# Kernel tuning notes

Hardware: AMD Instinct MI355X
Metric: run time of the kernel (lower is better)

## Reference

```python
import jax, jax.numpy as jnp
import numpy as np

K = 9        # kNN neighbors (ViG default kernel_size=9)
EPS = 1e-5   # BatchNorm eps


def _bn2d(x, gamma, beta):
    # training-mode BatchNorm2d over (B,H,W) per channel; x: [B,C,H,W]
    mean = jnp.mean(x, axis=(0, 2, 3), keepdims=True)
    var = jnp.var(x, axis=(0, 2, 3), keepdims=True)
    g = gamma.reshape(1, -1, 1, 1)
    b = beta.reshape(1, -1, 1, 1)
    return g * (x - mean) * jax.lax.rsqrt(var + EPS) + b


def setup_inputs() -> dict:
    key = jax.random.key(0)
    B, C, H, W = 8, 96, 56, 56
    oup = 192
    ks = jax.random.split(key, 8)
    sc = 0.05
    return {
        "x": jax.random.normal(ks[0], (B, C, H, W), dtype=jnp.float32),
        "W_fc1": jax.random.normal(ks[1], (C, C), dtype=jnp.float32) * sc,
        "b_fc1": jnp.zeros((C,), jnp.float32),
        "g_bn1": jnp.ones((C,), jnp.float32),
        "be_bn1": jnp.zeros((C,), jnp.float32),
        "W_edge": jax.random.normal(ks[2], (2 * C, 2 * C), dtype=jnp.float32) * sc,
        "b_edge": jnp.zeros((2 * C,), jnp.float32),
        "g_bne": jnp.ones((2 * C,), jnp.float32),
        "be_bne": jnp.zeros((2 * C,), jnp.float32),
        "W_fc2": jax.random.normal(ks[3], (2 * C, C), dtype=jnp.float32) * sc,
        "b_fc2": jnp.zeros((C,), jnp.float32),
        "g_bn2": jnp.ones((C,), jnp.float32),
        "be_bn2": jnp.zeros((C,), jnp.float32),
        "g_sabn": jnp.ones((C,), jnp.float32),
        "be_sabn": jnp.zeros((C,), jnp.float32),
        "W_dw": jax.random.normal(ks[4], (oup, C, 3, 3), dtype=jnp.float32) * sc,
        "b_dw": jnp.zeros((oup,), jnp.float32),
        "g_dwbn": jnp.ones((oup,), jnp.float32),
        "be_dwbn": jnp.zeros((oup,), jnp.float32),
    }


def reference(x, W_fc1, b_fc1, g_bn1, be_bn1, W_edge, b_edge, g_bne, be_bne,
              W_fc2, b_fc2, g_bn2, be_bn2, g_sabn, be_sabn,
              W_dw, b_dw, g_dwbn, be_dwbn):
    B, C, H, W = x.shape
    N = H * W
    shortcut = x

    # --- Grapher.fc1: 1x1 conv + BN ---
    y = jnp.einsum('bchw,cd->bdhw', x, W_fc1) + b_fc1[None, :, None, None]
    y = _bn2d(y, g_bn1, be_bn1)

    # --- dynamic kNN graph over flattened tokens ---
    ft = y.reshape(B, C, N).transpose(0, 2, 1)            # [B,N,C]
    sq = jnp.sum(ft * ft, axis=-1)                        # [B,N]
    dist = sq[:, :, None] - 2.0 * jnp.einsum('bnc,bmc->bnm', ft, ft) + sq[:, None, :]
    _, idx = jax.lax.top_k(-dist, K)                      # [B,N,K] nearest neighbors

    # --- EdgeConv: max_k act(BN(W [x_i, x_j - x_i])) ---
    x_j = jnp.take_along_axis(ft[:, :, None, :], idx[..., None], axis=1)  # [B,N,K,C]
    x_i = ft[:, :, None, :]                               # [B,N,1,C]
    e = jnp.concatenate([jnp.broadcast_to(x_i, x_j.shape), x_j - x_i], axis=-1)  # [B,N,K,2C]
    e = jnp.einsum('bnkc,cd->bnkd', e, W_edge) + b_edge
    m = jnp.mean(e, axis=(0, 1, 2))
    v = jnp.var(e, axis=(0, 1, 2))
    e = g_bne * (e - m) * jax.lax.rsqrt(v + EPS) + be_bne
    e = jax.nn.relu(e)
    g = jnp.max(e, axis=2)                                # [B,N,2C] max-aggregation

    # --- Grapher.fc2: 1x1 conv + BN, residual ---
    g = jnp.einsum('bnc,cd->bnd', g, W_fc2) + b_fc2       # [B,N,C]
    g = g.transpose(0, 2, 1).reshape(B, C, H, W)
    g = _bn2d(g, g_bn2, be_bn2)
    y = g + shortcut

    # --- SAEncoder: BN + ReLU ---
    y = jax.nn.relu(_bn2d(y, g_sabn, be_sabn))

    # --- convdw: 3x3 stride-2 conv + BN + ReLU ---
    y = jax.lax.conv_general_dilated(
        y, W_dw, window_strides=(2, 2), padding=((1, 1), (1, 1)),
        dimension_numbers=('NCHW', 'OIHW', 'NCHW')) + b_dw[None, :, None, None]
    y = jax.nn.relu(_bn2d(y, g_dwbn, be_dwbn))
    return y
```

## Files before the change

### kernel.cpp

```cpp
#include <hip/hip_runtime.h>
#include <math.h>

#define B_   8
#define C_   96
#define C2_  192
#define N_   3136
#define R_   25088
#define OUP_ 192
#define HO_  28
#define NO_  784
#define EPS_ 1e-5f
#define QS2  128
#define CAP3 64

typedef short bf16x8 __attribute__((ext_vector_type(8)));
typedef float f32x4  __attribute__((ext_vector_type(4)));

__device__ __forceinline__ int swz16(int i) { return (i & ~15) | ((i & 15) ^ ((i >> 4) & 7)); }

__global__ __launch_bounds__(512) void k_fc1_d(const float* __restrict__ x,
                                               const float* __restrict__ W1,
                                               const float* __restrict__ b1,
                                               double* __restrict__ yd) {
    __shared__ double Wl[96 * 48];
    int tid = threadIdx.x;
    int rl = tid & 255, h = tid >> 8;
    int dbase = blockIdx.y * 48;
    for (int q = tid; q < 96 * 48; q += 512) {
        int c = q / 48, dd = q % 48;
        Wl[c * 48 + dd] = (double)W1[c * 96 + dbase + dd];
    }
    __syncthreads();
    int r = blockIdx.x * 256 + rl;
    int b = r / N_;
    int n = r - b * N_;
    double acc[24];
#pragma unroll
    for (int i = 0; i < 24; i++) acc[i] = 0.0;
    const float* xp = x + (size_t)b * C_ * N_ + n;
    for (int c = 0; c < 96; ++c) {
        double xv = (double)xp[(size_t)c * N_];
        const double* w = &Wl[c * 48 + h * 24];
#pragma unroll
        for (int i = 0; i < 24; ++i) acc[i] += xv * w[i];
    }
    int d0 = dbase + h * 24;
#pragma unroll
    for (int i = 0; i < 24; i++) {
        int d = d0 + i;
        yd[((size_t)b * C_ + d) * N_ + n] = acc[i] + (double)b1[d];
    }
}

__global__ __launch_bounds__(256) void k_stats_chan_d(const double* __restrict__ src,
                                                      double* __restrict__ partial) {
    int c = blockIdx.x;
    int chunk = blockIdx.y;
    const int SPLIT = 16;
    double s = 0.0, ss = 0.0;
    for (int j = chunk * 256 + threadIdx.x; j < R_; j += SPLIT * 256) {
        int b = j / N_, n = j - b * N_;
        double v = src[((size_t)b * C_ + c) * N_ + n];
        s += v;
        ss += v * v;
    }
    __shared__ double red[8];
    for (int off = 32; off; off >>= 1) {
        s += __shfl_down(s, off, 64);
        ss += __shfl_down(ss, off, 64);
    }
    int lane = threadIdx.x & 63, w = threadIdx.x >> 6;
    if (lane == 0) { red[w * 2] = s; red[w * 2 + 1] = ss; }
    __syncthreads();
    if (threadIdx.x == 0) {
        s = red[0] + red[2] + red[4] + red[6];
        ss = red[1] + red[3] + red[5] + red[7];
        partial[(c * SPLIT + chunk) * 2] = s;
        partial[(c * SPLIT + chunk) * 2 + 1] = ss;
    }
}

__global__ void k_stats_reduce_d(const double* __restrict__ partial, double* __restrict__ stats) {
    int c = blockIdx.x * blockDim.x + threadIdx.x;
    if (c >= 96) return;
    double s = 0.0, ss = 0.0;
    for (int k = 0; k < 16; k++) {
        s += partial[(c * 16 + k) * 2];
        ss += partial[(c * 16 + k) * 2 + 1];
    }
    double m = s / (double)R_;
    double var = ss / (double)R_ - m * m;
    stats[c * 2] = m;
    stats[c * 2 + 1] = 1.0 / sqrt(var + 1e-5);
}

__global__ __launch_bounds__(256) void k_stats_chan(const float* __restrict__ src,
                                                    float* __restrict__ partial,
                                                    int Cn, int Nsp, int total) {
    int c = blockIdx.x;
    int chunk = blockIdx.y;
    int SPLIT = gridDim.y;
    float s = 0.f, ss = 0.f;
    for (int j = chunk * 256 + threadIdx.x; j < total; j += SPLIT * 256) {
        int b = j / Nsp, n = j - b * Nsp;
        float v = src[((size_t)b * Cn + c) * Nsp + n];
        s += v;
        ss += v * v;
    }
    __shared__ float red[8];
    for (int off = 32; off; off >>= 1) {
        s += __shfl_down(s, off, 64);
        ss += __shfl_down(ss, off, 64);
    }
    int lane = threadIdx.x & 63, w = threadIdx.x >> 6;
    if (lane == 0) { red[w * 2] = s; red[w * 2 + 1] = ss; }
    __syncthreads();
    if (threadIdx.x == 0) {
        s = red[0] + red[2] + red[4] + red[6];
        ss = red[1] + red[3] + red[5] + red[7];
        partial[(c * SPLIT + chunk) * 2] = s;
        partial[(c * SPLIT + chunk) * 2 + 1] = ss;
    }
}

__global__ void k_stats_reduce(const float* __restrict__ partial, float* __restrict__ stats,
                               int Cn, int SPLIT, float invcount) {
    int c = blockIdx.x * blockDim.x + threadIdx.x;
    if (c >= Cn) return;
    float s = 0.f, ss = 0.f;
    for (int k = 0; k < SPLIT; k++) {
        s += partial[(c * SPLIT + k) * 2];
        ss += partial[(c * SPLIT + k) * 2 + 1];
    }
    float m = s * invcount;
    float var = ss * invcount - m * m;
    stats[c * 2] = m;
    stats[c * 2 + 1] = 1.0f / sqrtf(var + EPS_);
}

__global__ __launch_bounds__(256) void k_stats_reduce_b2(const float* __restrict__ partial,
                                                         float* __restrict__ stats,
                                                         float invcount) {
    int c = blockIdx.x;
    float s = 0.f, ss = 0.f;
    for (int k = threadIdx.x; k < 784; k += 256) {
        s  += partial[(size_t)k * 384 + c];
        ss += partial[(size_t)k * 384 + 192 + c];
    }
    __shared__ float red[8];
    for (int off = 32; off; off >>= 1) {
        s += __shfl_down(s, off, 64);
        ss += __shfl_down(ss, off, 64);
    }
    int lane = threadIdx.x & 63, w = threadIdx.x >> 6;
    if (lane == 0) { red[w * 2] = s; red[w * 2 + 1] = ss; }
    __syncthreads();
    if (threadIdx.x == 0) {
        s = red[0] + red[2] + red[4] + red[6];
        ss = red[1] + red[3] + red[5] + red[7];
        float m = s * invcount;
        float var = ss * invcount - m * m;
        stats[c * 2] = m;
        stats[c * 2 + 1] = 1.0f / sqrtf(var + EPS_);
    }
}

__global__ __launch_bounds__(256) void k_bn1_tr(const double* __restrict__ yd,
                                                const double* __restrict__ stats,
                                                const float* __restrict__ g,
                                                const float* __restrict__ be,
                                                float* __restrict__ ftc,
                                                double* __restrict__ ftp64,
                                                unsigned short* __restrict__ fspH,
                                                double* __restrict__ sq64,
                                                float* __restrict__ sq32) {
    __shared__ double tile[64 * 97];
    __shared__ double dsq[64][4];
    int b = blockIdx.y;
    int n0 = blockIdx.x * 64;
    int tid = threadIdx.x;
    int n = tid & 63, w = tid >> 6;
    for (int k = 0; k < 24; ++k) {
        int c = k * 4 + w;
        size_t gi = ((size_t)b * C_ + c) * N_ + n0 + n;
        double m = stats[c * 2], rs = stats[c * 2 + 1];
        double v = (double)g[c] * (yd[gi] - m) * rs + (double)be[c];
        ftc[gi] = (float)v;
        tile[n * 97 + c] = v;
    }
    __syncthreads();
    int p = n, q = w;
    double vals[24];
    double s = 0.0;
    const double* lp = &tile[p * 97 + q * 24];
#pragma unroll
    for (int m2 = 0; m2 < 24; ++m2) { vals[m2] = lp[m2]; s += vals[m2] * vals[m2]; }
    dsq[p][q] = s;
    double* dst = ftp64 + ((size_t)b * N_ + n0 + p) * C_ + q * 24;
#pragma unroll
    for (int m2 = 0; m2 < 24; m2 += 2) *(double2*)&dst[m2] = make_double2(vals[m2], vals[m2 + 1]);
    unsigned* hdst = (unsigned*)(fspH + ((size_t)b * N_ + n0 + p) * QS2);
#pragma unroll
    for (int m2 = 0; m2 < 24; m2 += 2) {
        unsigned u0 = __float_as_uint((float)vals[m2]);
        unsigned u1 = __float_as_uint((float)vals[m2 + 1]);
        unsigned h0 = (u0 + 0x7fffu + ((u0 >> 16) & 1u)) >> 16;
        unsigned h1 = (u1 + 0x7fffu + ((u1 >> 16) & 1u)) >> 16;
        hdst[q * 12 + (m2 >> 1)] = h0 | (h1 << 16);
    }
    __syncthreads();
    if (tid < 64) {
        double tot = dsq[tid][0] + dsq[tid][1] + dsq[tid][2] + dsq[tid][3];
        sq64[(size_t)b * N_ + n0 + tid] = tot;
        sq32[(size_t)b * N_ + n0 + tid] = (float)tot;
    }
}

__global__ __launch_bounds__(256) void k_dist3(const unsigned short* __restrict__ fspH,
                                               const float* __restrict__ sq32,
                                               unsigned short* __restrict__ poolC,
                                               unsigned* __restrict__ poolCnt) {
    __shared__ __align__(16) char lds[48256];
    unsigned short* cminL = (unsigned short*)(lds + 32768);
    unsigned short* poolL = (unsigned short*)(lds + 39040);
    unsigned*       cntL  = (unsigned*)(lds + 47232);
    float*          t9fL  = (float*)(lds + 47488);

    int b = blockIdx.y;
    int q0 = blockIdx.x * 64;
    int tid = threadIdx.x;
    int w = tid >> 6, l = tid & 63;

    {
        const uint4* src = (const uint4*)(fspH + ((size_t)b * N_ + q0) * QS2);
        uint4* dst = (uint4*)lds;
        for (int i = tid; i < 1024; i += 256) dst[swz16(i)] = src[i];
    }
    __syncthreads();
    bf16x8 Bq[3];
    {
        const unsigned short* Ql = (const unsigned short*)lds;
        int qr = w * 16 + (l & 15);
#pragma unroll
        for (int s = 0; s < 3; ++s) {
            int col = (s * 4 + (l >> 4)) ^ (qr & 7);
            Bq[s] = *(const bf16x8*)&Ql[qr * QS2 + col * 8];
        }
    }
    __syncthreads();

    {
        const uint4* src = (const uint4*)(fspH + (size_t)b * N_ * QS2);
        uint4* dst = (uint4*)lds;
        for (int i = tid; i < 1024; i += 256) dst[swz16(i)] = src[i];
        if (tid < 64) ((float*)(lds + 47744))[tid] = sq32[(size_t)b * N_ + tid];
    }
    __syncthreads();

    float t9r = 0.f;
    int cur = 0;
    for (int t = 0; t < 98; ++t) {
        int ch = (t < 49) ? t : t - 49;
        int c0 = ch * 64;
        bool pf = (t < 97);
        uint4 st0, st1, st2, st3; float sqst = 0.f;
        if (pf) {
            int nch = (t + 1 < 49) ? (t + 1) : (t + 1 - 49);
            const uint4* src = (const uint4*)(fspH + ((size_t)b * N_ + nch * 64) * QS2);
            st0 = src[tid];
            st1 = src[tid + 256];
            st2 = src[tid + 512];
            st3 = src[tid + 768];
            if (tid < 64) sqst = sq32[(size_t)b * N_ + nch * 64 + tid];
        }
        const unsigned short* Bc = (const unsigned short*)(lds + cur * 16384);
        const float* sqc = (const float*)(lds + 47744 + cur * 256);
        f32x4 acc[4];
#pragma unroll
        for (int ct = 0; ct < 4; ++ct) acc[ct] = (f32x4){0.f, 0.f, 0.f, 0.f};
#pragma unroll
        for (int s = 0; s < 3; ++s) {
#pragma unroll
            for (int ct = 0; ct < 4; ++ct) {
                int cr = ct * 16 + (l & 15);
                int col = (s * 4 + (l >> 4)) ^ (cr & 7);
                bf16x8 Ac = *(const bf16x8*)&Bc[cr * QS2 + col * 8];
                acc[ct] = __builtin_amdgcn_mfma_f32_16x16x32_bf16(Ac, Bq[s], acc[ct], 0, 0, 0);
            }
        }
        f32x4 scn[4];
#pragma unroll
        for (int ct = 0; ct < 4; ++ct) scn[ct] = *(const f32x4*)&sqc[ct * 16 + (l >> 4) * 4];
        if (t < 49) {
            float m = 1e30f;
#pragma unroll
            for (int ct = 0; ct < 4; ++ct)
#pragma unroll
                for (int j = 0; j < 4; ++j)
                    m = fminf(m, fmaf(-2.f, acc[ct][j], scn[ct][j]));
            m = fminf(m, __shfl_xor(m, 16, 64));
            m = fminf(m, __shfl_xor(m, 32, 64));
            if (l < 16) {
                unsigned u = __float_as_uint(m);
                unsigned ku = u ^ (0x80000000u | (unsigned)((int)u >> 31));
                cminL[ch * 64 + w * 16 + l] = (unsigned short)(ku >> 16);
            }
        } else {
            int qrow = w * 16 + (l & 15);
#pragma unroll
            for (int ct = 0; ct < 4; ++ct)
#pragma unroll
                for (int j = 0; j < 4; ++j) {
                    float d = fmaf(-2.f, acc[ct][j], scn[ct][j]);
                    if (d <= t9r) {
                        unsigned pos = atomicAdd(&cntL[qrow], 1u);
                        if (pos < (unsigned)CAP3)
                            poolL[qrow * CAP3 + pos] = (unsigned short)(c0 + ct * 16 + (l >> 4) * 4 + j);
                    }
                }
        }
        if (t == 48) {
            __syncthreads();
            if (tid < 64) {
                unsigned short top[9];
#pragma unroll
                for (int j = 0; j < 9; ++j) top[j] = 0xFFFFu;
                for (int q = 0; q < 49; ++q) {
                    unsigned short v = cminL[q * 64 + tid];
                    if (v < top[8]) {
                        top[8] = v;
#pragma unroll
                        for (int j = 8; j >= 1; --j)
                            if (top[j] < top[j - 1]) { unsigned short tt = top[j]; top[j] = top[j - 1]; top[j - 1] = tt; }
                    }
                }
                unsigned ku = ((unsigned)top[8] << 16) | 0xFFFFu;
                float f = (ku & 0x80000000u) ? __uint_as_float(ku ^ 0x80000000u)
                                             : __uint_as_float(~ku);
                t9fL[tid] = f + fabsf(f) * 0.01f + 1.0f;
                cntL[tid] = 0u;
            }
            __syncthreads();
            t9r = t9fL[w * 16 + (l & 15)];
        }
        if (pf) {
            uint4* dst = (uint4*)(lds + (cur ^ 1) * 16384);
            dst[swz16(tid)] = st0;
            dst[swz16(tid + 256)] = st1;
            dst[swz16(tid + 512)] = st2;
            dst[swz16(tid + 768)] = st3;
            if (tid < 64) ((float*)(lds + 47744 + (cur ^ 1) * 256))[tid] = sqst;
        }
        __syncthreads();
        cur ^= 1;
    }
    if (tid < 64) {
        unsigned c = cntL[tid];
        poolCnt[(size_t)b * N_ + q0 + tid] = (c > (unsigned)CAP3) ? (unsigned)CAP3 : c;
    }
    {
        unsigned* dst = (unsigned*)(poolC + ((size_t)b * N_ + q0) * CAP3);
        const unsigned* src = (const unsigned*)poolL;
        for (int i = tid; i < 64 * CAP3 / 2; i += 256) dst[i] = src[i];
    }
}

__global__ __launch_bounds__(256) void k_rerank_d(const unsigned short* __restrict__ poolC,
                                                  const unsigned* __restrict__ poolCnt,
                                                  const double* __restrict__ ftp64,
                                                  const double* __restrict__ sq64,
                                                  int* __restrict__ idx) {
    int tid = threadIdx.x;
    int wv = tid >> 6, l = tid & 63;
    int rr = blockIdx.x * 4 + wv;
    int b = rr / N_;
    int cnt = (int)poolCnt[rr];
    if (cnt > CAP3) cnt = CAP3;
    int e = l & 3;
    double qreg[24];
    {
        const double* qb = ftp64 + (size_t)rr * C_ + e * 24;
#pragma unroll
        for (int m = 0; m < 24; ++m) qreg[m] = qb[m];
    }
    double dv[4];
    int jv[4];
#pragma unroll
    for (int gG = 0; gG < 4; ++gG) { dv[gG] = 1e300; jv[gG] = 0x7fffffff; }
#pragma unroll
    for (int gG = 0; gG < 4; ++gG) {
        if (gG * 16 >= cnt) break;
        int ci = gG * 16 + (l >> 2);
        bool valid = ci < cnt;
        int j = valid ? (int)poolC[(size_t)rr * CAP3 + ci] : 0;
        const double* cb = ftp64 + ((size_t)b * N_ + j) * C_ + e * 24;
        double p = 0.0;
#pragma unroll
        for (int m = 0; m < 24; ++m) p += qreg[m] * cb[m];
        p += __shfl_xor(p, 1, 64);
        p += __shfl_xor(p, 2, 64);
        if (valid) {
            dv[gG] = sq64[(size_t)b * N_ + j] - 2.0 * p;
            jv[gG] = j;
        }
    }
#pragma unroll
    for (int r = 0; r < 9; ++r) {
        double dm = dv[0]; int jm = jv[0];
#pragma unroll
        for (int gG = 1; gG < 4; ++gG)
            if (dv[gG] < dm || (dv[gG] == dm && jv[gG] < jm)) { dm = dv[gG]; jm = jv[gG]; }
#pragma unroll
        for (int off = 1; off <= 32; off <<= 1) {
            double od = __shfl_xor(dm, off, 64);
            int oj = __shfl_xor(jm, off, 64);
            if (od < dm || (od == dm && oj < jm)) { dm = od; jm = oj; }
        }
        if (l == 0) idx[(size_t)rr * 9 + r] = jm;
#pragma unroll
        for (int gG = 0; gG < 4; ++gG)
            if (jv[gG] == jm) dv[gG] = 1e300;
    }
}

__global__ __launch_bounds__(512) void k_gemm_uv(const float* __restrict__ ftc,
                                                 const float* __restrict__ We,
                                                 const float* __restrict__ beb,
                                                 float* __restrict__ out, int mode) {
    __shared__ float Wl[96 * 48];
    int tid = threadIdx.x;
    int rl = tid & 255, h = tid >> 8;
    int dbase = blockIdx.y * 48;
    for (int q = tid; q < 96 * 48; q += 512) {
        int c = q / 48, dd = q % 48;
        float w = We[(96 + c) * C2_ + dbase + dd];
        if (mode == 0) w = We[c * C2_ + dbase + dd] - w;
        Wl[c * 48 + dd] = w;
    }
    __syncthreads();
    int r = blockIdx.x * 256 + rl;
    int b = r / N_, n = r - b * N_;
    float acc[24];
#pragma unroll
    for (int i = 0; i < 24; i++) acc[i] = 0.f;
    const float* xp = ftc + (size_t)b * C_ * N_ + n;
    for (int c = 0; c < 96; ++c) {
        float xv = xp[(size_t)c * N_];
        const float4* w4 = (const float4*)&Wl[c * 48 + h * 24];
#pragma unroll
        for (int i = 0; i < 6; ++i) {
            float4 w = w4[i];
            acc[i * 4 + 0] += xv * w.x;
            acc[i * 4 + 1] += xv * w.y;
            acc[i * 4 + 2] += xv * w.z;
            acc[i * 4 + 3] += xv * w.w;
        }
    }
    int d0 = dbase + h * 24;
    float* op = out + (size_t)r * C2_ + d0;
#pragma unroll
    for (int i = 0; i < 6; ++i) {
        float4 o;
        o.x = acc[i * 4 + 0]; o.y = acc[i * 4 + 1];
        o.z = acc[i * 4 + 2]; o.w = acc[i * 4 + 3];
        if (mode == 0) {
            o.x += beb[d0 + i * 4 + 0];
            o.y += beb[d0 + i * 4 + 1];
            o.z += beb[d0 + i * 4 + 2];
            o.w += beb[d0 + i * 4 + 3];
        }
        ((float4*)op)[i] = o;
    }
}

__global__ __launch_bounds__(192) void k_bne_stats(const float* __restrict__ u,
                                                   const float* __restrict__ v,
                                                   const int* __restrict__ idx,
                                                   float* __restrict__ partial) {
    int d = threadIdx.x;
    int row0 = blockIdx.x * 32;
    int b = row0 / N_;
    float s = 0.f, ss = 0.f;
    for (int r = 0; r < 32; ++r) {
        int row = row0 + r;
        float ud = u[(size_t)row * C2_ + d];
        const int* ip = idx + (size_t)row * 9;
#pragma unroll
        for (int k = 0; k < 9; k++) {
            int j = ip[k];
            float e = ud + v[((size_t)b * N_ + j) * C2_ + d];
            s += e;
            ss += e * e;
        }
    }
    partial[(size_t)blockIdx.x * 384 + d] = s;
    partial[(size_t)blockIdx.x * 384 + 192 + d] = ss;
}

__global__ __launch_bounds__(192) void k_edge_fc2(const float* __restrict__ u,
                                                  const float* __restrict__ v,
                                                  const int* __restrict__ idx,
                                                  const float* __restrict__ statsE,
                                                  const float* __restrict__ ge,
                                                  const float* __restrict__ bee,
                                                  const float* __restrict__ W2,
                                                  const float* __restrict__ b2,
                                                  float* __restrict__ out2) {
    __shared__ float gl[16][C2_];
    __shared__ float g2[C_][16];
    int tid = threadIdx.x;
    int row0 = blockIdx.x * 16;
    int b = row0 / N_;
    int n0 = row0 - b * N_;
    {
        int d = tid;
        float m = statsE[d * 2], rs = statsE[d * 2 + 1];
        float ga = ge[d], bb = bee[d];
        for (int r = 0; r < 16; ++r) {
            int row = row0 + r;
            float ud = u[(size_t)row * C2_ + d];
            const int* ip = idx + (size_t)row * 9;
            float gm = 0.f;
#pragma unroll
            for (int k = 0; k < 9; k++) {
                int j = ip[k];
                float e = ud + v[((size_t)b * N_ + j) * C2_ + d];
                float val = ga * (e - m) * rs + bb;
                gm = fmaxf(gm, val);
            }
            gl[r][d] = gm;
        }
    }
    __syncthreads();
    {
        int rr = tid / 24;
        int dq = tid % 24;
        for (int rep = 0; rep < 2; ++rep) {
            int r = rr + rep * 8;
            float4 acc = *(const float4*)&b2[dq * 4];
            for (int d = 0; d < C2_; ++d) {
                float gv = gl[r][d];
                float4 w = *(const float4*)&W2[d * C_ + dq * 4];
                acc.x += gv * w.x;
                acc.y += gv * w.y;
                acc.z += gv * w.z;
                acc.w += gv * w.w;
            }
            g2[dq * 4 + 0][r] = acc.x;
            g2[dq * 4 + 1][r] = acc.y;
            g2[dq * 4 + 2][r] = acc.z;
            g2[dq * 4 + 3][r] = acc.w;
        }
    }
    __syncthreads();
    for (int q = tid; q < 96 * 4; q += 192) {
        int dd = q / 4, part = q % 4;
        float4 val = *(const float4*)&g2[dd][part * 4];
        *(float4*)&out2[((size_t)b * C_ + dd) * N_ + n0 + part * 4] = val;
    }
}

__global__ __launch_bounds__(256) void k_bn2_add_st(const float* __restrict__ out2,
                                                    const float* __restrict__ x,
                                                    const float* __restrict__ stats,
                                                    const float* __restrict__ g,
                                                    const float* __restrict__ be,
                                                    float* __restrict__ t,
                                                    float* __restrict__ partial) {
    int c = blockIdx.x;
    int chunk = blockIdx.y;
    const int SPLIT = 16;
    float m = stats[c * 2], rs = stats[c * 2 + 1];
    float ga = g[c], bb = be[c];
    float s = 0.f, ss = 0.f;
    for (int j = chunk * 256 + threadIdx.x; j < R_; j += SPLIT * 256) {
        int b = j / N_, n = j - b * N_;
        size_t i = ((size_t)b * C_ + c) * N_ + n;
        float tv = ga * (out2[i] - m) * rs + bb + x[i];
        t[i] = tv;
        s += tv;
        ss += tv * tv;
    }
    __shared__ float red[8];
    for (int off = 32; off; off >>= 1) {
        s += __shfl_down(s, off, 64);
        ss += __shfl_down(ss, off, 64);
    }
    int lane = threadIdx.x & 63, w = threadIdx.x >> 6;
    if (lane == 0) { red[w * 2] = s; red[w * 2 + 1] = ss; }
    __syncthreads();
    if (threadIdx.x == 0) {
        s = red[0] + red[2] + red[4] + red[6];
        ss = red[1] + red[3] + red[5] + red[7];
        partial[(c * SPLIT + chunk) * 2] = s;
        partial[(c * SPLIT + chunk) * 2 + 1] = ss;
    }
}

__global__ __launch_bounds__(256) void k_sabn_relu(const float* __restrict__ t,
                                                   const float* __restrict__ stats,
                                                   const float* __restrict__ g,
                                                   const float* __restrict__ be,
                                                   float* __restrict__ s) {
    int i = blockIdx.x * 256 + threadIdx.x;
    if (i >= B_ * C_ * N_) return;
    int c = (i / N_) % C_;
    s[i] = fmaxf(g[c] * (t[i] - stats[c * 2]) * stats[c * 2 + 1] + be[c], 0.f);
}

__global__ __launch_bounds__(256) void k_conv(const float* __restrict__ s,
                                              const float* __restrict__ Wd,
                                              const float* __restrict__ bd,
                                              float* __restrict__ z) {
    __shared__ float Wl[96 * 9 * 16];
    int b = blockIdx.z;
    int oc0 = blockIdx.y * 16;
    int p = blockIdx.x * 256 + threadIdx.x;
    for (int i = threadIdx.x; i < 96 * 9 * 16; i += 256) {
        int oc = i & 15;
        int icq = i >> 4;
        Wl[i] = Wd[(size_t)(oc0 + oc) * 864 + icq];
    }
    __syncthreads();
    if (p >= NO_) return;
    int oh = p / HO_, ow = p % HO_;
    float acc[16];
#pragma unroll
    for (int i = 0; i < 16; i++) acc[i] = 0.f;
    int ih0 = oh * 2 - 1, iw0 = ow * 2 - 1;
    const float* sb = s + (size_t)b * C_ * N_;
    for (int ic = 0; ic < 96; ++ic) {
        const float* sp = sb + (size_t)ic * N_;
        float in[9];
#pragma unroll
        for (int kh = 0; kh < 3; kh++) {
            int ih = ih0 + kh;
            bool okh = (unsigned)ih < 56u;
#pragma unroll
            for (int kw = 0; kw < 3; kw++) {
                int iw = iw0 + kw;
                bool ok = okh && ((unsigned)iw < 56u);
                in[kh * 3 + kw] = ok ? sp[ih * 56 + iw] : 0.f;
            }
        }
#pragma unroll
        for (int q = 0; q < 9; q++) {
            float iv = in[q];
            const float4* w4 = (const float4*)&Wl[(ic * 9 + q) * 16];
#pragma unroll
            for (int j = 0; j < 4; j++) {
                float4 w = w4[j];
                acc[j * 4 + 0] += iv * w.x;
                acc[j * 4 + 1] += iv * w.y;
                acc[j * 4 + 2] += iv * w.z;
                acc[j * 4 + 3] += iv * w.w;
            }
        }
    }
#pragma unroll
    for (int i = 0; i < 16; i++)
        z[((size_t)b * OUP_ + oc0 + i) * NO_ + p] = acc[i] + bd[oc0 + i];
}

__global__ __launch_bounds__(256) void k_out(const float* __restrict__ z,
                                             const float* __restrict__ stats,
                                             const float* __restrict__ g,
                                             const float* __restrict__ be,
                                             float* __restrict__ out) {
    int i = blockIdx.x * 256 + threadIdx.x;
    if (i >= B_ * OUP_ * NO_) return;
    int c = (i / NO_) % OUP_;
    out[i] = fmaxf(g[c] * (z[i] - stats[c * 2]) * stats[c * 2 + 1] + be[c], 0.f);
}

extern "C" void kernel_launch(void* const* d_in, const int* in_sizes, int n_in,
                              void* d_out, int out_size, void* d_ws, size_t ws_size,
                              hipStream_t stream) {
    const float* x     = (const float*)d_in[0];
    const float* W_fc1 = (const float*)d_in[1];
    const float* b_fc1 = (const float*)d_in[2];
    const float* g_bn1 = (const float*)d_in[3];
    const float* be_bn1= (const float*)d_in[4];
    const float* W_edge= (const float*)d_in[5];
    const float* b_edge= (const float*)d_in[6];
    const float* g_bne = (const float*)d_in[7];
    const float* be_bne= (const float*)d_in[8];
    const float* W_fc2 = (const float*)d_in[9];
    const float* b_fc2 = (const float*)d_in[10];
    const float* g_bn2 = (const float*)d_in[11];
    const float* be_bn2= (const float*)d_in[12];
    const float* g_sabn= (const float*)d_in[13];
    const float* be_sabn=(const float*)d_in[14];
    const float* W_dw  = (const float*)d_in[15];
    const float* b_dw  = (const float*)d_in[16];
    const float* g_dwbn= (const float*)d_in[17];
    const float* be_dwbn=(const float*)d_in[18];

    char* base = (char*)d_ws;
    float*  ftc   = (float*)(base + 0);
    float*  sbuf  = (float*)(base + 0);
    double* ftp64 = (double*)(base + 9633792);
    float*  uu    = (float*)(base + 9633792);
    double* yd    = (double*)(base + 28901376);
    float*  vv    = (float*)(base + 28901376);
    unsigned short* fspH = (unsigned short*)(base + 48168960);
    float*  out2  = (float*)(base + 48168960);
    unsigned short* poolC = (unsigned short*)(base + 57802752);
    float*  tbuf  = (float*)(base + 57802752);
    double* sq64  = (double*)(base + 67436544);
    int*    idx   = (int*)(base + 67637248);
    unsigned* poolCnt = (unsigned*)(base + 68540416);
    float*  sq32  = (float*)(base + 68640768);
    float*  partial = (float*)(base + 68741120);
    double* partiald = (double*)(base + 68741120);
    double* stats1d = (double*)(base + 69945344);
    float*  statsE  = (float*)(base + 69946880);
    float*  stats2  = (float*)(base + 69948416);
    float*  statsS  = (float*)(base + 69949952);
    float*  statsD  = (float*)(base + 69951488);
    float*  zbuf  = (float*)(base + 69953024);

    k_fc1_d<<<dim3(98, 2), 512, 0, stream>>>(x, W_fc1, b_fc1, yd);
    k_stats_chan_d<<<dim3(96, 16), 256, 0, stream>>>(yd, partiald);
    k_stats_reduce_d<<<1, 256, 0, stream>>>(partiald, stats1d);
    k_bn1_tr<<<dim3(49, B_), 256, 0, stream>>>(yd, stats1d, g_bn1, be_bn1, ftc, ftp64, fspH, sq64, sq32);

    k_dist3<<<dim3(49, B_), 256, 0, stream>>>(fspH, sq32, poolC, poolCnt);
    k_rerank_d<<<6272, 256, 0, stream>>>(poolC, poolCnt, ftp64, sq64, idx);

    k_gemm_uv<<<dim3(98, 4), 512, 0, stream>>>(ftc, W_edge, b_edge, uu, 0);
    k_gemm_uv<<<dim3(98, 4), 512, 0, stream>>>(ftc, W_edge, b_edge, vv, 1);

    k_bne_stats<<<784, 192, 0, stream>>>(uu, vv, idx, partial);
    k_stats_reduce_b2<<<192, 256, 0, stream>>>(partial, statsE, 1.0f / 225792.0f);
    k_edge_fc2<<<1568, 192, 0, stream>>>(uu, vv, idx, statsE, g_bne, be_bne, W_fc2, b_fc2, out2);

    k_stats_chan<<<dim3(96, 16), 256, 0, stream>>>(out2, partial, 96, N_, R_);
    k_stats_reduce<<<1, 256, 0, stream>>>(partial, stats2, 96, 16, 1.0f / (float)R_);
    k_bn2_add_st<<<dim3(96, 16), 256, 0, stream>>>(out2, x, stats2, g_bn2, be_bn2, tbuf, partial);
    k_stats_reduce<<<1, 256, 0, stream>>>(partial, statsS, 96, 16, 1.0f / (float)R_);
    k_sabn_relu<<<9408, 256, 0, stream>>>(tbuf, statsS, g_sabn, be_sabn, sbuf);

    k_conv<<<dim3(4, 12, 8), 256, 0, stream>>>(sbuf, W_dw, b_dw, zbuf);
    k_stats_chan<<<dim3(192, 8), 256, 0, stream>>>(zbuf, partial, 192, NO_, 6272);
    k_stats_reduce<<<1, 256, 0, stream>>>(partial, statsD, 192, 8, 1.0f / 6272.0f);
    k_out<<<4705, 256, 0, stream>>>(zbuf, statsD, g_dwbn, be_dwbn, (float*)d_out);
}
```

Baseline: 570.7 us.

## Split kNN distance pass into min/threshold/compare kernels and fuse u/v GEMMs

```diff
diff --git a/kernel.cpp b/kernel.cpp
--- a/kernel.cpp
+++ b/kernel.cpp
@@ -172,8 +172,7 @@
                                                 float* __restrict__ ftc,
                                                 double* __restrict__ ftp64,
                                                 unsigned short* __restrict__ fspH,
-                                                double* __restrict__ sq64,
-                                                float* __restrict__ sq32) {
+                                                double* __restrict__ sq64) {
     __shared__ double tile[64 * 97];
     __shared__ double dsq[64][4];
     int b = blockIdx.y;
@@ -212,74 +211,67 @@
     if (tid < 64) {
         double tot = dsq[tid][0] + dsq[tid][1] + dsq[tid][2] + dsq[tid][3];
         sq64[(size_t)b * N_ + n0 + tid] = tot;
-        sq32[(size_t)b * N_ + n0 + tid] = (float)tot;
-    }
-}
-
-__global__ __launch_bounds__(256) void k_dist3(const unsigned short* __restrict__ fspH,
-                                               const float* __restrict__ sq32,
-                                               unsigned short* __restrict__ poolC,
-                                               unsigned* __restrict__ poolCnt) {
-    __shared__ __align__(16) char lds[48256];
-    unsigned short* cminL = (unsigned short*)(lds + 32768);
-    unsigned short* poolL = (unsigned short*)(lds + 39040);
-    unsigned*       cntL  = (unsigned*)(lds + 47232);
-    float*          t9fL  = (float*)(lds + 47488);
-
-    int b = blockIdx.y;
+        float t32 = (float)(-0.5 * tot);
+        unsigned u0 = __float_as_uint(t32);
+        unsigned h0 = (u0 + 0x7fffu + ((u0 >> 16) & 1u)) >> 16;
+        float resid = t32 - __uint_as_float(h0 << 16);
+        unsigned u1 = __float_as_uint(resid);
+        unsigned h1 = (u1 + 0x7fffu + ((u1 >> 16) & 1u)) >> 16;
+        unsigned* hd = (unsigned*)(fspH + ((size_t)b * N_ + n0 + tid) * QS2);
+        hd[48] = h0 | (h1 << 16);
+#pragma unroll
+        for (int k2 = 49; k2 < 64; ++k2) hd[k2] = 0u;
+    }
+}
+
+__global__ __launch_bounds__(256) void k_dist_min(const unsigned short* __restrict__ fspH,
+                                                  unsigned short* __restrict__ cminG) {
+    __shared__ __align__(16) char lds[32768];
+    int b = blockIdx.z, half = blockIdx.y;
     int q0 = blockIdx.x * 64;
-    int tid = threadIdx.x;
-    int w = tid >> 6, l = tid & 63;
+    int tid = threadIdx.x, w = tid >> 6, l = tid & 63;
+    int ch0 = half * 25;
+    int nch = half ? 24 : 25;
+    const int koff = (l >> 4) * 8;
 
     {
-        const uint4* src = (const uint4*)(fspH + ((size_t)b * N_ + q0) * QS2);
-        uint4* dst = (uint4*)lds;
-        for (int i = tid; i < 1024; i += 256) dst[swz16(i)] = src[i];
-    }
-    __syncthreads();
-    bf16x8 Bq[3];
+        const uint4* qsrc = (const uint4*)(fspH + ((size_t)b * N_ + q0) * QS2);
+        const uint4* csrc = (const uint4*)(fspH + ((size_t)b * N_ + ch0 * 64) * QS2);
+        uint4* qb = (uint4*)(lds + 16384);
+        uint4* cb = (uint4*)lds;
+        for (int i = tid; i < 1024; i += 256) { qb[swz16(i)] = qsrc[i]; cb[swz16(i)] = csrc[i]; }
+    }
+    __syncthreads();
+    bf16x8 Bq[4];
     {
-        const unsigned short* Ql = (const unsigned short*)lds;
+        const unsigned short* Ql = (const unsigned short*)(lds + 16384);
         int qr = w * 16 + (l & 15);
 #pragma unroll
         for (int s = 0; s < 3; ++s) {
             int col = (s * 4 + (l >> 4)) ^ (qr & 7);
             Bq[s] = *(const bf16x8*)&Ql[qr * QS2 + col * 8];
         }
-    }
-    __syncthreads();
-
-    {
-        const uint4* src = (const uint4*)(fspH + (size_t)b * N_ * QS2);
-        uint4* dst = (uint4*)lds;
-        for (int i = tid; i < 1024; i += 256) dst[swz16(i)] = src[i];
-        if (tid < 64) ((float*)(lds + 47744))[tid] = sq32[(size_t)b * N_ + tid];
-    }
-    __syncthreads();
-
-    float t9r = 0.f;
+        bf16x8 z = {0, 0, 0, 0, 0, 0, 0, 0};
+        if ((l >> 4) == 0) { z[0] = (short)0x3F80; z[1] = (short)0x3F80; }
+        Bq[3] = z;
+    }
+    __syncthreads();
+
     int cur = 0;
-    for (int t = 0; t < 98; ++t) {
-        int ch = (t < 49) ? t : t - 49;
-        int c0 = ch * 64;
-        bool pf = (t < 97);
-        uint4 st0, st1, st2, st3; float sqst = 0.f;
+    for (int t = 0; t < nch; ++t) {
+        int chg = ch0 + t;
+        bool pf = (t < nch - 1);
+        uint4 st0, st1, st2, st3;
         if (pf) {
-            int nch = (t + 1 < 49) ? (t + 1) : (t + 1 - 49);
-            const uint4* src = (const uint4*)(fspH + ((size_t)b * N_ + nch * 64) * QS2);
-            st0 = src[tid];
-            st1 = src[tid + 256];
-            st2 = src[tid + 512];
-            st3 = src[tid + 768];
-            if (tid < 64) sqst = sq32[(size_t)b * N_ + nch * 64 + tid];
+            const uint4* src = (const uint4*)(fspH + ((size_t)b * N_ + (chg + 1) * 64) * QS2);
+            st0 = src[tid]; st1 = src[tid + 256]; st2 = src[tid + 512]; st3 = src[tid + 768];
         }
         const unsigned short* Bc = (const unsigned short*)(lds + cur * 16384);
-        const float* sqc = (const float*)(lds + 47744 + cur * 256);
         f32x4 acc[4];
 #pragma unroll
         for (int ct = 0; ct < 4; ++ct) acc[ct] = (f32x4){0.f, 0.f, 0.f, 0.f};
 #pragma unroll
-        for (int s = 0; s < 3; ++s) {
+        for (int s = 0; s < 4; ++s) {
 #pragma unroll
             for (int ct = 0; ct < 4; ++ct) {
                 int cr = ct * 16 + (l & 15);
@@ -288,60 +280,18 @@
                 acc[ct] = __builtin_amdgcn_mfma_f32_16x16x32_bf16(Ac, Bq[s], acc[ct], 0, 0, 0);
             }
         }
-        f32x4 scn[4];
-#pragma unroll
-        for (int ct = 0; ct < 4; ++ct) scn[ct] = *(const f32x4*)&sqc[ct * 16 + (l >> 4) * 4];
-        if (t < 49) {
-            float m = 1e30f;
-#pragma unroll
-            for (int ct = 0; ct < 4; ++ct)
-#pragma unroll
-                for (int j = 0; j < 4; ++j)
-                    m = fminf(m, fmaf(-2.f, acc[ct][j], scn[ct][j]));
-            m = fminf(m, __shfl_xor(m, 16, 64));
-            m = fminf(m, __shfl_xor(m, 32, 64));
-            if (l < 16) {
-                unsigned u = __float_as_uint(m);
-                unsigned ku = u ^ (0x80000000u | (unsigned)((int)u >> 31));
-                cminL[ch * 64 + w * 16 + l] = (unsigned short)(ku >> 16);
-            }
-        } else {
-            int qrow = w * 16 + (l & 15);
-#pragma unroll
-            for (int ct = 0; ct < 4; ++ct)
-#pragma unroll
-                for (int j = 0; j < 4; ++j) {
-                    float d = fmaf(-2.f, acc[ct][j], scn[ct][j]);
-                    if (d <= t9r) {
-                        unsigned pos = atomicAdd(&cntL[qrow], 1u);
-                        if (pos < (unsigned)CAP3)
-                            poolL[qrow * CAP3 + pos] = (unsigned short)(c0 + ct * 16 + (l >> 4) * 4 + j);
-                    }
-                }
-        }
-        if (t == 48) {
-            __syncthreads();
-            if (tid < 64) {
-                unsigned short top[9];
-#pragma unroll
-                for (int j = 0; j < 9; ++j) top[j] = 0xFFFFu;
-                for (int q = 0; q < 49; ++q) {
-                    unsigned short v = cminL[q * 64 + tid];
-                    if (v < top[8]) {
-                        top[8] = v;
-#pragma unroll
-                        for (int j = 8; j >= 1; --j)
-                            if (top[j] < top[j - 1]) { unsigned short tt = top[j]; top[j] = top[j - 1]; top[j - 1] = tt; }
-                    }
-                }
-                unsigned ku = ((unsigned)top[8] << 16) | 0xFFFFu;
-                float f = (ku & 0x80000000u) ? __uint_as_float(ku ^ 0x80000000u)
-                                             : __uint_as_float(~ku);
-                t9fL[tid] = f + fabsf(f) * 0.01f + 1.0f;
-                cntL[tid] = 0u;
-            }
-            __syncthreads();
-            t9r = t9fL[w * 16 + (l & 15)];
+        float mx = -1e30f;
+#pragma unroll
+        for (int ct = 0; ct < 4; ++ct)
+#pragma unroll
+            for (int j = 0; j < 4; ++j) mx = fmaxf(mx, acc[ct][j]);
+        mx = fmaxf(mx, __shfl_xor(mx, 16, 64));
+        mx = fmaxf(mx, __shfl_xor(mx, 32, 64));
+        if (l < 16) {
+            float dmin = -2.f * mx;
+            unsigned u = __float_as_uint(dmin);
+            unsigned ku = u ^ (0x80000000u | (unsigned)((int)u >> 31));
+            cminG[((size_t)(b * N_ + q0 + w * 16 + l)) * 49 + chg] = (unsigned short)(ku >> 16);
         }
         if (pf) {
             uint4* dst = (uint4*)(lds + (cur ^ 1) * 16384);
@@ -349,19 +299,117 @@
             dst[swz16(tid + 256)] = st1;
             dst[swz16(tid + 512)] = st2;
             dst[swz16(tid + 768)] = st3;
-            if (tid < 64) ((float*)(lds + 47744 + (cur ^ 1) * 256))[tid] = sqst;
         }
         __syncthreads();
         cur ^= 1;
     }
-    if (tid < 64) {
-        unsigned c = cntL[tid];
-        poolCnt[(size_t)b * N_ + q0 + tid] = (c > (unsigned)CAP3) ? (unsigned)CAP3 : c;
-    }
+}
+
+__global__ __launch_bounds__(256) void k_t9(const unsigned short* __restrict__ cminG,
+                                            float* __restrict__ thr2f,
+                                            unsigned* __restrict__ poolCnt) {
+    int q = blockIdx.x * 256 + threadIdx.x;
+    if (q >= R_) return;
+    const unsigned short* p = cminG + (size_t)q * 49;
+    unsigned short top[9];
+#pragma unroll
+    for (int j = 0; j < 9; ++j) top[j] = 0xFFFFu;
+    for (int i = 0; i < 49; ++i) {
+        unsigned short v = p[i];
+        if (v < top[8]) {
+            top[8] = v;
+#pragma unroll
+            for (int j = 8; j >= 1; --j)
+                if (top[j] < top[j - 1]) { unsigned short tt = top[j]; top[j] = top[j - 1]; top[j - 1] = tt; }
+        }
+    }
+    unsigned ku = ((unsigned)top[8] << 16) | 0xFFFFu;
+    float f = (ku & 0x80000000u) ? __uint_as_float(ku ^ 0x80000000u) : __uint_as_float(~ku);
+    float t9 = f + fabsf(f) * 0.008f + 0.75f;
+    thr2f[q] = -0.5f * t9;
+    poolCnt[q] = 0u;
+}
+
+__global__ __launch_bounds__(256) void k_dist_cmp(const unsigned short* __restrict__ fspH,
+                                                  const float* __restrict__ thr2f,
+                                                  unsigned short* __restrict__ poolC,
+                                                  unsigned* __restrict__ poolCnt) {
+    __shared__ __align__(16) char lds[32768];
+    int b = blockIdx.z, half = blockIdx.y;
+    int q0 = blockIdx.x * 64;
+    int tid = threadIdx.x, w = tid >> 6, l = tid & 63;
+    int ch0 = half * 25;
+    int nch = half ? 24 : 25;
+    const int koff = (l >> 4) * 8;
+    int qg = b * N_ + q0 + w * 16 + (l & 15);
+    float thr2r = thr2f[qg];
+
     {
-        unsigned* dst = (unsigned*)(poolC + ((size_t)b * N_ + q0) * CAP3);
-        const unsigned* src = (const unsigned*)poolL;
-        for (int i = tid; i < 64 * CAP3 / 2; i += 256) dst[i] = src[i];
+        const uint4* qsrc = (const uint4*)(fspH + ((size_t)b * N_ + q0) * QS2);
+        const uint4* csrc = (const uint4*)(fspH + ((size_t)b * N_ + ch0 * 64) * QS2);
+        uint4* qb = (uint4*)(lds + 16384);
+        uint4* cb = (uint4*)lds;
+        for (int i = tid; i < 1024; i += 256) { qb[swz16(i)] = qsrc[i]; cb[swz16(i)] = csrc[i]; }
+    }
+    __syncthreads();
+    bf16x8 Bq[4];
+    {
+        const unsigned short* Ql = (const unsigned short*)(lds + 16384);
+        int qr = w * 16 + (l & 15);
+#pragma unroll
+        for (int s = 0; s < 3; ++s) {
+            int col = (s * 4 + (l >> 4)) ^ (qr & 7);
+            Bq[s] = *(const bf16x8*)&Ql[qr * QS2 + col * 8];
+        }
+        bf16x8 z = {0, 0, 0, 0, 0, 0, 0, 0};
+        if ((l >> 4) == 0) { z[0] = (short)0x3F80; z[1] = (short)0x3F80; }
+        Bq[3] = z;
+    }
+    __syncthreads();
+
+    int cur = 0;
+    for (int t = 0; t < nch; ++t) {
+        int chg = ch0 + t;
+        int c0 = chg * 64;
+        bool pf = (t < nch - 1);
+        uint4 st0, st1, st2, st3;
+        if (pf) {
+            const uint4* src = (const uint4*)(fspH + ((size_t)b * N_ + (chg + 1) * 64) * QS2);
+            st0 = src[tid]; st1 = src[tid + 256]; st2 = src[tid + 512]; st3 = src[tid + 768];
+        }
+        const unsigned short* Bc = (const unsigned short*)(lds + cur * 16384);
+        f32x4 acc[4];
+#pragma unroll
+        for (int ct = 0; ct < 4; ++ct) acc[ct] = (f32x4){0.f, 0.f, 0.f, 0.f};
+#pragma unroll
+        for (int s = 0; s < 4; ++s) {
+#pragma unroll
+            for (int ct = 0; ct < 4; ++ct) {
+                int cr = ct * 16 + (l & 15);
+                int col = (s * 4 + (l >> 4)) ^ (cr & 7);
+                bf16x8 Ac = *(const bf16x8*)&Bc[cr * QS2 + col * 8];
+                acc[ct] = __builtin_amdgcn_mfma_f32_16x16x32_bf16(Ac, Bq[s], acc[ct], 0, 0, 0);
+            }
+        }
+#pragma unroll
+        for (int ct = 0; ct < 4; ++ct)
+#pragma unroll
+            for (int j = 0; j < 4; ++j) {
+                if (acc[ct][j] >= thr2r) {
+                    unsigned pos = atomicAdd(&poolCnt[qg], 1u);
+                    if (pos < (unsigned)CAP3)
+                        poolC[(size_t)qg * CAP3 + pos] = (unsigned short)(c0 + ct * 16 + (l >> 4) * 4 + j);
+                }
+            }
+        if (pf) {
+            uint4* dst = (uint4*)(lds + (cur ^ 1) * 16384);
+            dst[swz16(tid)] = st0;
+            dst[swz16(tid + 256)] = st1;
+            dst[swz16(tid + 512)] = st2;
+            dst[swz16(tid + 768)] = st3;
+        }
+        __syncthreads();
+        cur ^= 1;
     }
 }
 
@@ -423,53 +471,55 @@
     }
 }
 
-__global__ __launch_bounds__(512) void k_gemm_uv(const float* __restrict__ ftc,
-                                                 const float* __restrict__ We,
-                                                 const float* __restrict__ beb,
-                                                 float* __restrict__ out, int mode) {
-    __shared__ float Wl[96 * 48];
+__global__ __launch_bounds__(512) void k_gemm_uv2(const float* __restrict__ ftc,
+                                                  const float* __restrict__ We,
+                                                  const float* __restrict__ beb,
+                                                  float* __restrict__ u,
+                                                  float* __restrict__ v) {
+    __shared__ float Wl[2][96 * 48];
     int tid = threadIdx.x;
     int rl = tid & 255, h = tid >> 8;
     int dbase = blockIdx.y * 48;
     for (int q = tid; q < 96 * 48; q += 512) {
         int c = q / 48, dd = q % 48;
-        float w = We[(96 + c) * C2_ + dbase + dd];
-        if (mode == 0) w = We[c * C2_ + dbase + dd] - w;
-        Wl[c * 48 + dd] = w;
+        float wb = We[(96 + c) * C2_ + dbase + dd];
+        Wl[1][q] = wb;
+        Wl[0][q] = We[c * C2_ + dbase + dd] - wb;
     }
     __syncthreads();
     int r = blockIdx.x * 256 + rl;
     int b = r / N_, n = r - b * N_;
-    float acc[24];
-#pragma unroll
-    for (int i = 0; i < 24; i++) acc[i] = 0.f;
+    float a0[24], a1[24];
+#pragma unroll
+    for (int i = 0; i < 24; i++) { a0[i] = 0.f; a1[i] = 0.f; }
     const float* xp = ftc + (size_t)b * C_ * N_ + n;
     for (int c = 0; c < 96; ++c) {
         float xv = xp[(size_t)c * N_];
-        const float4* w4 = (const float4*)&Wl[c * 48 + h * 24];
+        const float4* w40 = (const float4*)&Wl[0][c * 48 + h * 24];
+        const float4* w41 = (const float4*)&Wl[1][c * 48 + h * 24];
 #pragma unroll
         for (int i = 0; i < 6; ++i) {
-            float4 w = w4[i];
-            acc[i * 4 + 0] += xv * w.x;
-            acc[i * 4 + 1] += xv * w.y;
-            acc[i * 4 + 2] += xv * w.z;
-            acc[i * 4 + 3] += xv * w.w;
+            float4 w0 = w40[i], w1 = w41[i];
+            a0[i * 4 + 0] += xv * w0.x; a0[i * 4 + 1] += xv * w0.y;
+            a0[i * 4 + 2] += xv * w0.z; a0[i * 4 + 3] += xv * w0.w;
+            a1[i * 4 + 0] += xv * w1.x; a1[i * 4 + 1] += xv * w1.y;
+            a1[i * 4 + 2] += xv * w1.z; a1[i * 4 + 3] += xv * w1.w;
         }
     }
     int d0 = dbase + h * 24;
-    float* op = out + (size_t)r * C2_ + d0;
+    float* up = u + (size_t)r * C2_ + d0;
+    float* vp = v + (size_t)r * C2_ + d0;
 #pragma unroll
     for (int i = 0; i < 6; ++i) {
-        float4 o;
-        o.x = acc[i * 4 + 0]; o.y = acc[i * 4 + 1];
-        o.z = acc[i * 4 + 2]; o.w = acc[i * 4 + 3];
-        if (mode == 0) {
-            o.x += beb[d0 + i * 4 + 0];
-            o.y += beb[d0 + i * 4 + 1];
-            o.z += beb[d0 + i * 4 + 2];
-            o.w += beb[d0 + i * 4 + 3];
-        }
-        ((float4*)op)[i] = o;
+        float4 ou, ov;
+        ou.x = a0[i * 4 + 0] + beb[d0 + i * 4 + 0];
+        ou.y = a0[i * 4 + 1] + beb[d0 + i * 4 + 1];
+        ou.z = a0[i * 4 + 2] + beb[d0 + i * 4 + 2];
+        ou.w = a0[i * 4 + 3] + beb[d0 + i * 4 + 3];
+        ov.x = a1[i * 4 + 0]; ov.y = a1[i * 4 + 1];
+        ov.z = a1[i * 4 + 2]; ov.w = a1[i * 4 + 3];
+        ((float4*)up)[i] = ou;
+        ((float4*)vp)[i] = ov;
     }
 }
 
@@ -710,7 +760,7 @@
     double* sq64  = (double*)(base + 67436544);
     int*    idx   = (int*)(base + 67637248);
     unsigned* poolCnt = (unsigned*)(base + 68540416);
-    float*  sq32  = (float*)(base + 68640768);
+    float*  thr2f = (float*)(base + 68640768);
     float*  partial = (float*)(base + 68741120);
     double* partiald = (double*)(base + 68741120);
     double* stats1d = (double*)(base + 69945344);
@@ -719,17 +769,19 @@
     float*  statsS  = (float*)(base + 69949952);
     float*  statsD  = (float*)(base + 69951488);
     float*  zbuf  = (float*)(base + 69953024);
+    unsigned short* cminG = (unsigned short*)(base + 69953024);
 
     k_fc1_d<<<dim3(98, 2), 512, 0, stream>>>(x, W_fc1, b_fc1, yd);
     k_stats_chan_d<<<dim3(96, 16), 256, 0, stream>>>(yd, partiald);
     k_stats_reduce_d<<<1, 256, 0, stream>>>(partiald, stats1d);
-    k_bn1_tr<<<dim3(49, B_), 256, 0, stream>>>(yd, stats1d, g_bn1, be_bn1, ftc, ftp64, fspH, sq64, sq32);
-
-    k_dist3<<<dim3(49, B_), 256, 0, stream>>>(fspH, sq32, poolC, poolCnt);
+    k_bn1_tr<<<dim3(49, B_), 256, 0, stream>>>(yd, stats1d, g_bn1, be_bn1, ftc, ftp64, fspH, sq64);
+
+    k_dist_min<<<dim3(49, 2, B_), 256, 0, stream>>>(fspH, cminG);
+    k_t9<<<98, 256, 0, stream>>>(cminG, thr2f, poolCnt);
+    k_dist_cmp<<<dim3(49, 2, B_), 256, 0, stream>>>(fspH, thr2f, poolC, poolCnt);
     k_rerank_d<<<6272, 256, 0, stream>>>(poolC, poolCnt, ftp64, sq64, idx);
 
-    k_gemm_uv<<<dim3(98, 4), 512, 0, stream>>>(ftc, W_edge, b_edge, uu, 0);
-    k_gemm_uv<<<dim3(98, 4), 512, 0, stream>>>(ftc, W_edge, b_edge, vv, 1);
+    k_gemm_uv2<<<dim3(98, 4), 512, 0, stream>>>(ftc, W_edge, b_edge, uu, vv);
 
     k_bne_stats<<<784, 192, 0, stream>>>(uu, vv, idx, partial);
     k_stats_reduce_b2<<<192, 256, 0, stream>>>(partial, statsE, 1.0f / 225792.0f);
```

Result: slower. 590.4 us (+3.4%).
